# Kernel optimization log

Measured on AMD Instinct MI355X. Metric: run time of the kernel, lower is better.

Reference implementation:

```python
import jax, jax.numpy as jnp
import numpy as np

NUM_GROUPS = 32
EPS = 1e-6


def group_norm(x, gamma, beta):
    b, c, h, w = x.shape
    xg = x.reshape(b, NUM_GROUPS, c // NUM_GROUPS, h, w)
    mean = jnp.mean(xg, axis=(2, 3, 4), keepdims=True)
    var = jnp.var(xg, axis=(2, 3, 4), keepdims=True)
    xg = (xg - mean) * jax.lax.rsqrt(var + EPS)
    x = xg.reshape(b, c, h, w)
    return x * gamma[None, :, None, None] + beta[None, :, None, None]


def conv1x1(x, w, b):
    # x: [B,C,H,W], w: [Cout,Cin], b: [Cout]
    return jnp.einsum('bchw,oc->bohw', x, w) + b[None, :, None, None]


def setup_inputs() -> dict:
    key = jax.random.key(0)
    ks = jax.random.split(key, 11)
    B, C, H, W = 2, 512, 64, 64
    s = 1.0 / np.sqrt(C)
    return {
        'x': jax.random.normal(ks[0], (B, C, H, W), jnp.float32),
        'norm_gamma': jnp.ones((C,), jnp.float32),
        'norm_beta': jnp.zeros((C,), jnp.float32),
        'wq': jax.random.normal(ks[1], (C, C), jnp.float32) * s,
        'bq': jnp.zeros((C,), jnp.float32),
        'wk': jax.random.normal(ks[2], (C, C), jnp.float32) * s,
        'bk': jnp.zeros((C,), jnp.float32),
        'wv': jax.random.normal(ks[3], (C, C), jnp.float32) * s,
        'bv': jnp.zeros((C,), jnp.float32),
        'wo': jax.random.normal(ks[4], (C, C), jnp.float32) * s,
        'bo': jnp.zeros((C,), jnp.float32),
    }


def reference(x, norm_gamma, norm_beta, wq, bq, wk, bk, wv, bv, wo, bo):
    b, c, h, w = x.shape
    hn = group_norm(x, norm_gamma, norm_beta)
    q = conv1x1(hn, wq, bq).reshape(b, c, h * w)  # [B,C,HW]
    k = conv1x1(hn, wk, bk).reshape(b, c, h * w)
    v = conv1x1(hn, wv, bv).reshape(b, c, h * w)
    scale = jnp.asarray(c, x.dtype) ** -0.5
    # scores[b,i,j] = sum_c q[b,c,i] * k[b,c,j]
    scores = jnp.einsum('bci,bcj->bij', q, k) * scale
    attn = jax.nn.softmax(scores, axis=2)
    # out[b,c,i] = sum_j v[b,c,j] * attn[b,i,j]
    out = jnp.einsum('bcj,bij->bci', v, attn).reshape(b, c, h, w)
    out = conv1x1(out, wo, bo)
    return x + out
```

## Files before the change

kernel.cpp:

```cpp
#include <hip/hip_runtime.h>
#include <hip/hip_bf16.h>

using u16 = unsigned short;
typedef __attribute__((ext_vector_type(4))) float f32x4;
typedef __attribute__((ext_vector_type(8))) __bf16 bf16x8;
typedef __attribute__((ext_vector_type(8))) short s16x8;
typedef __attribute__((ext_vector_type(4))) short s16x4;

#define DEVI __device__ __forceinline__

constexpr int BATCH = 2, C = 512, HW = 4096, NG = 32, CPG = 16;

DEVI float b2f(u16 u) { union { unsigned u; float f; } a; a.u = ((unsigned)u) << 16; return a.f; }
DEVI u16 f2b(float f) {
  union { float f; unsigned u; } a; a.f = f;
  unsigned r = a.u + 0x7fffu + ((a.u >> 16) & 1u);
  return (u16)(r >> 16);
}

DEVI void xcd_remap(int& bx, int& by, int& bz) {
  const int nx = gridDim.x, ny = gridDim.y;
  const int nwg = nx * ny * gridDim.z;
  const int flat = blockIdx.x + nx * (blockIdx.y + ny * blockIdx.z);
  const int cpx = nwg >> 3;
  const int w = (flat & 7) * cpx + (flat >> 3);
  bx = w % nx;
  const int t = w / nx;
  by = t % ny;
  bz = t / ny;
}

__global__ __launch_bounds__(256) void cvt_w(const float* __restrict__ a, const float* __restrict__ b,
                                             const float* __restrict__ c, const float* __restrict__ d,
                                             u16* __restrict__ out) {
  int i = blockIdx.x * 256 + threadIdx.x;
  int w = i >> 16;
  int off = (i & 65535) * 4;
  const float* s = (w == 0) ? a : (w == 1) ? b : (w == 2) ? c : d;
  f32x4 v = *(const f32x4*)(s + off);
  s16x4 o;
  o[0] = (short)f2b(v[0]); o[1] = (short)f2b(v[1]); o[2] = (short)f2b(v[2]); o[3] = (short)f2b(v[3]);
  *(s16x4*)(out + (size_t)w * 262144 + off) = o;
}

__global__ __launch_bounds__(1024) void gn_stats(const float* __restrict__ x, float* __restrict__ stats) {
  int bg = blockIdx.x;
  const f32x4* xg = (const f32x4*)(x + (size_t)bg * (CPG * HW));
  float s = 0.f, ss = 0.f;
  for (int i = threadIdx.x; i < CPG * HW / 4; i += 1024) {
    f32x4 v = xg[i];
    s += v[0] + v[1] + v[2] + v[3];
    ss += v[0] * v[0] + v[1] * v[1] + v[2] * v[2] + v[3] * v[3];
  }
  #pragma unroll
  for (int o = 32; o; o >>= 1) { s += __shfl_xor(s, o); ss += __shfl_xor(ss, o); }
  __shared__ float red[32];
  int wv = threadIdx.x >> 6, ln = threadIdx.x & 63;
  if (ln == 0) { red[wv] = s; red[16 + wv] = ss; }
  __syncthreads();
  if (threadIdx.x == 0) {
    float S = 0.f, SS = 0.f;
    for (int i = 0; i < 16; ++i) { S += red[i]; SS += red[16 + i]; }
    float inv = 1.f / (float)(CPG * HW);
    float mean = S * inv;
    float var = SS * inv - mean * mean;
    stats[bg * 2] = mean;
    stats[bg * 2 + 1] = rsqrtf(var + 1e-6f);
  }
}

__global__ __launch_bounds__(256) void gn_normT(const float* __restrict__ x, const float* __restrict__ stats,
                                                const float* __restrict__ gamma, const float* __restrict__ beta,
                                                u16* __restrict__ hnT) {
  __shared__ u16 tile[64][66];
  int b = blockIdx.z, c0 = blockIdx.y * 64, h0 = blockIdx.x * 64;
  int t = threadIdx.x;
  const float* xb = x + ((size_t)b * C + c0) * HW + h0;
  int r = t / 16, cc = (t % 16) * 4;
  #pragma unroll
  for (int it = 0; it < 4; ++it) {
    int rr = it * 16 + r;
    int ch = c0 + rr;
    int g = b * NG + (ch >> 4);
    float mean = stats[g * 2], rstd = stats[g * 2 + 1];
    float ga = gamma[ch] * rstd;
    float be = beta[ch] - mean * ga;
    f32x4 v = *(const f32x4*)(xb + (size_t)rr * HW + cc);
    #pragma unroll
    for (int j = 0; j < 4; ++j) tile[rr][cc + j] = f2b(v[j] * ga + be);
  }
  __syncthreads();
  u16* op = hnT + (size_t)b * HW * C + (size_t)h0 * C + c0;
  int hr2 = t / 8, cg = (t % 8) * 8;
  #pragma unroll
  for (int it = 0; it < 2; ++it) {
    int hr = it * 32 + hr2;
    s16x8 o8;
    #pragma unroll
    for (int j = 0; j < 8; ++j) o8[j] = (short)tile[cg + j][hr];
    *(s16x8*)(op + (size_t)hr * C + cg) = o8;
  }
}

#define EPI_BIAS_M 1
#define EPI_BIAS_N 2
#define EPI_RESID  4
#define EPI_F32OUT 8
#define EPI_QK     32

template <int EPI>
__global__ __launch_bounds__(256) void gemm_bt(const u16* __restrict__ A, const u16* __restrict__ Bt,
                                               void* __restrict__ Co, int M, int N, int K,
                                               long long sA, long long sB, long long sC,
                                               const float* __restrict__ bias,
                                               const float* __restrict__ biasB,
                                               const float* __restrict__ resid, long long sR) {
  (void)M;
  __shared__ u16 ldsA[128 * 64];
  __shared__ u16 ldsB[128 * 64];
  const int tid = threadIdx.x;
  int bn, bm, bz;
  xcd_remap(bn, bm, bz);
  A += (size_t)bz * sA;
  Bt += (size_t)bz * sB;
  const int wave = tid >> 6, lane = tid & 63;
  const int wr = wave >> 1, wc = wave & 1;
  f32x4 acc[4][4] = {};

  const int srow = tid >> 3;
  const int sch = (tid & 7) ^ (srow & 7);
  const u16* gA = A + (size_t)(bm * 128 + srow) * K + sch * 8;
  const u16* gB = Bt + (size_t)(bn * 128 + srow) * K + sch * 8;
  u16* lA = ldsA + wave * 512;
  u16* lB = ldsB + wave * 512;

  for (int k0 = 0; k0 < K; k0 += 64) {
    #pragma unroll
    for (int cc = 0; cc < 4; ++cc) {
      __builtin_amdgcn_global_load_lds(
          (const __attribute__((address_space(1))) void*)(gA + (size_t)cc * 32 * K + k0),
          (__attribute__((address_space(3))) void*)(lA + cc * 2048), 16, 0, 0);
      __builtin_amdgcn_global_load_lds(
          (const __attribute__((address_space(1))) void*)(gB + (size_t)cc * 32 * K + k0),
          (__attribute__((address_space(3))) void*)(lB + cc * 2048), 16, 0, 0);
    }
    __syncthreads();
    #pragma unroll
    for (int kk = 0; kk < 2; ++kk) {
      bf16x8 af[4], bfv[4];
      #pragma unroll
      for (int m = 0; m < 4; ++m) {
        int r = wr * 64 + m * 16 + (lane & 15);
        int chunk = (kk * 4 + (lane >> 4)) ^ (r & 7);
        af[m] = *(const bf16x8*)(ldsA + r * 64 + chunk * 8);
      }
      #pragma unroll
      for (int n = 0; n < 4; ++n) {
        int r = wc * 64 + n * 16 + (lane & 15);
        int chunk = (kk * 4 + (lane >> 4)) ^ (r & 7);
        bfv[n] = *(const bf16x8*)(ldsB + r * 64 + chunk * 8);
      }
      #pragma unroll
      for (int m = 0; m < 4; ++m)
        #pragma unroll
        for (int n = 0; n < 4; ++n)
          acc[m][n] = __builtin_amdgcn_mfma_f32_16x16x32_bf16(af[m], bfv[n], acc[m][n], 0, 0, 0);
    }
    __syncthreads();
  }

  const int col0 = bn * 128 + wc * 64;
  const int row0 = bm * 128 + wr * 64 + ((lane >> 4) << 2);
  #pragma unroll
  for (int m = 0; m < 4; ++m) {
    #pragma unroll
    for (int j = 0; j < 4; ++j) {
      int gm = row0 + m * 16 + j;
      float bm_v = (EPI & EPI_BIAS_M) ? bias[gm] : 0.f;
      #pragma unroll
      for (int n = 0; n < 4; ++n) {
        int gn = col0 + n * 16 + (lane & 15);
        float v = acc[m][n][j] + bm_v;
        if (EPI & EPI_BIAS_N) {
          if (EPI & EPI_QK) v += (gn < 512) ? bias[gn] : biasB[gn - 512];
          else v += bias[gn];
        }
        if (EPI & EPI_RESID) v += resid[(size_t)bz * sR + (size_t)gm * N + gn];
        if (EPI & EPI_F32OUT)
          ((float*)Co)[(size_t)bz * sC + (size_t)gm * N + gn] = v;
        else
          ((u16*)Co)[(size_t)bz * sC + (size_t)gm * N + gn] = f2b(v);
      }
    }
  }
}

template <bool SCALED>
__global__ __launch_bounds__(512, 2) void gemm256(
    const u16* __restrict__ Ag, const u16* __restrict__ Bg,
    u16* __restrict__ Co, u16* __restrict__ Co2, int zSwitch,
    int Nld, int ldK, int nsplitLog, int kLen,
    long long sA, long long sB, long long sC, float scale) {
  __shared__ u16 lds[65536];
  const int tid = threadIdx.x;
  const int lane = tid & 63, w = tid >> 6;
  const int wm = w >> 2, wn = w & 3;
  const int l15 = lane & 15, l4 = lane >> 4;
  int bn, bm, z;
  xcd_remap(bn, bm, z);
  const int bz = z >> nsplitLog, kz = z & ((1 << nsplitLog) - 1);
  const int kStart = kz * kLen;
  const int NT = kLen >> 6;

  const int rStage = w * 8 + (lane >> 3);
  const int gch = (lane & 7) ^ (lane >> 3);
  const u16* gA = Ag + (size_t)bz * sA + (size_t)(bm * 256) * ldK + kStart + gch * 8;
  const u16* gB = Bg + (size_t)bz * sB + (size_t)(bn * 256) * ldK + kStart + gch * 8;

  f32x4 acc[8][4] = {};
  bf16x8 aF[4][2], bF[2][2][2];

  const int hB = wn >> 1, qB = wn & 1;
  const u16* pA0 = lds + (0 * 4 + wm) * 8192;
  const u16* pA1 = lds + (1 * 4 + wm) * 8192;
  const u16* pB0 = lds + (0 * 4 + 2 + hB) * 8192;
  const u16* pB1 = lds + (1 * 4 + 2 + hB) * 8192;

  #define STAGE(TT, DB, AB, HF) { \
    const u16* gbase = (AB) ? gB : gA; \
    u16* l0 = lds + ((DB) * 4 + (AB) * 2 + (HF)) * 8192 + w * 512; \
    _Pragma("unroll") for (int s = 0; s < 2; ++s) { \
      const u16* gp = gbase + (size_t)((HF) * 128 + s * 64 + rStage) * ldK + (TT) * 64; \
      __builtin_amdgcn_global_load_lds((const __attribute__((address_space(1))) void*)gp, \
          (__attribute__((address_space(3))) void*)(l0 + s * 4096), 16, 0, 0); } }

  #define LOAD_A(P, MH) { _Pragma("unroll") for (int j = 0; j < 4; ++j) \
    _Pragma("unroll") for (int kk = 0; kk < 2; ++kk) { \
      const int r_ = (MH) * 64 + j * 16 + l15; const int c_ = (kk * 4 + l4) ^ (r_ & 7); \
      aF[j][kk] = *(const bf16x8*)((P) + r_ * 64 + c_ * 8); } }

  #define LOAD_B(P, NH) { _Pragma("unroll") for (int j = 0; j < 2; ++j) \
    _Pragma("unroll") for (int kk = 0; kk < 2; ++kk) { \
      const int r_ = qB * 64 + (NH) * 32 + j * 16 + l15; const int c_ = (kk * 4 + l4) ^ (r_ & 7); \
      bF[NH][j][kk] = *(const bf16x8*)((P) + r_ * 64 + c_ * 8); } }

  #define MM(MH, NH) { __builtin_amdgcn_s_setprio(1); \
    _Pragma("unroll") for (int j = 0; j < 4; ++j) \
      _Pragma("unroll") for (int j2 = 0; j2 < 2; ++j2) \
        _Pragma("unroll") for (int kk = 0; kk < 2; ++kk) \
          acc[(MH) * 4 + j][(NH) * 2 + j2] = __builtin_amdgcn_mfma_f32_16x16x32_bf16( \
              aF[j][kk], bF[NH][j2][kk], acc[(MH) * 4 + j][(NH) * 2 + j2], 0, 0, 0); \
    __builtin_amdgcn_s_setprio(0); }

  #define BAR __builtin_amdgcn_s_barrier()
  #define WLG { asm volatile("s_waitcnt lgkmcnt(0)" ::: "memory"); __builtin_amdgcn_sched_barrier(0); }
  #define WV4 asm volatile("s_waitcnt vmcnt(4)" ::: "memory")
  #define WV0 asm volatile("s_waitcnt vmcnt(0)" ::: "memory")

  STAGE(0, 0, 1, 0); STAGE(0, 0, 1, 1);
  STAGE(0, 0, 0, 0); STAGE(0, 0, 0, 1);
  STAGE(1, 1, 1, 0); STAGE(1, 1, 1, 1);
  WV4; BAR;

  const int NI = NT / 2 - 1;
  for (int i = 0; i < NI; ++i) {
    const int t1 = 2 * i + 1, u0 = 2 * i + 2, u1 = 2 * i + 3;
    LOAD_A(pA0, 0); LOAD_B(pB0, 0); STAGE(t1, 1, 0, 0); BAR; WLG; MM(0, 0); BAR;
    LOAD_B(pB0, 1); STAGE(t1, 1, 0, 1); BAR; WLG; MM(0, 1); BAR;
    LOAD_A(pA0, 1); STAGE(u0, 0, 1, 0); BAR; WLG; MM(1, 1); BAR;
    STAGE(u0, 0, 1, 1); BAR; WLG; MM(1, 0); WV4; BAR;
    LOAD_A(pA1, 0); LOAD_B(pB1, 0); STAGE(u0, 0, 0, 0); BAR; WLG; MM(0, 0); BAR;
    LOAD_B(pB1, 1); STAGE(u0, 0, 0, 1); BAR; WLG; MM(0, 1); BAR;
    LOAD_A(pA1, 1); STAGE(u1, 1, 1, 0); BAR; WLG; MM(1, 1); BAR;
    STAGE(u1, 1, 1, 1); BAR; WLG; MM(1, 0); WV4; BAR;
  }
  {
    const int t1 = NT - 1;
    LOAD_A(pA0, 0); LOAD_B(pB0, 0); STAGE(t1, 1, 0, 0); BAR; WLG; MM(0, 0); BAR;
    LOAD_B(pB0, 1); STAGE(t1, 1, 0, 1); BAR; WLG; MM(0, 1); BAR;
    LOAD_A(pA0, 1); BAR; WLG; MM(1, 1); BAR;
    BAR; WLG; MM(1, 0); WV0; BAR;
    LOAD_A(pA1, 0); LOAD_B(pB1, 0); BAR; WLG; MM(0, 0); BAR;
    LOAD_B(pB1, 1); BAR; WLG; MM(0, 1); BAR;
    LOAD_A(pA1, 1); BAR; WLG; MM(1, 1); BAR;
    MM(1, 0);
  }
  #undef STAGE
  #undef LOAD_A
  #undef LOAD_B
  #undef MM
  #undef BAR
  #undef WLG
  #undef WV4
  #undef WV0

  {
    const int rloc = wm * 128 + l4 * 4;
    const int cloc = wn * 64 + l15;
    #pragma unroll
    for (int m = 0; m < 8; ++m) {
      #pragma unroll
      for (int j = 0; j < 4; ++j) {
        const int r_ = rloc + m * 16 + j;
        const int xr = ((r_ >> 2) & 3) << 5;
        #pragma unroll
        for (int n = 0; n < 4; ++n) {
          float v = acc[m][n][j];
          if (SCALED) v *= scale;
          *(u16*)((char*)lds + ((r_ * 512 + (cloc + n * 16) * 2) ^ xr)) = f2b(v);
        }
      }
    }
    __syncthreads();
    u16* outp = (z < zSwitch) ? (Co + (size_t)z * sC) : (Co2 + (size_t)(z - zSwitch) * sC);
    #pragma unroll
    for (int it = 0; it < 16; ++it) {
      const int idx = it * 512 + tid;
      const int r_ = idx >> 5, ch = idx & 31;
      const int xr = ((r_ >> 2) & 3) << 5;
      s16x8 d8 = *(const s16x8*)((const char*)lds + ((r_ * 512 + ch * 16) ^ xr));
      *(s16x8*)(outp + (size_t)(bm * 256 + r_) * Nld + bn * 256 + ch * 8) = d8;
    }
  }
}

__global__ __launch_bounds__(256) void softmax_rows(u16* __restrict__ S) {
  int row = blockIdx.x * 4 + (threadIdx.x >> 6);
  int lane = threadIdx.x & 63;
  s16x8* p = (s16x8*)(S + (size_t)row * 4096);
  float v[64];
  float m = -1e30f;
  #pragma unroll
  for (int j = 0; j < 8; ++j) {
    s16x8 raw = p[j * 64 + lane];
    #pragma unroll
    for (int e = 0; e < 8; ++e) {
      float f = b2f((u16)raw[e]);
      v[j * 8 + e] = f;
      m = fmaxf(m, f);
    }
  }
  #pragma unroll
  for (int o = 32; o; o >>= 1) m = fmaxf(m, __shfl_xor(m, o));
  float s = 0.f;
  #pragma unroll
  for (int i = 0; i < 64; ++i) { v[i] = __expf(v[i] - m); s += v[i]; }
  #pragma unroll
  for (int o = 32; o; o >>= 1) s += __shfl_xor(s, o);
  float r = 1.f / s;
  #pragma unroll
  for (int j = 0; j < 8; ++j) {
    s16x8 o8;
    #pragma unroll
    for (int e = 0; e < 8; ++e) o8[e] = (short)f2b(v[j * 8 + e] * r);
    p[j * 64 + lane] = o8;
  }
}

__global__ __launch_bounds__(256) void reduce_pv(const u16* __restrict__ P, const u16* __restrict__ P2,
                                                 u16* __restrict__ ao) {
  const size_t e = ((size_t)blockIdx.x * 256 + threadIdx.x) * 8;
  const int b = (int)(e >> 21);
  const size_t o = e & 2097151;
  float s[8] = {0.f, 0.f, 0.f, 0.f, 0.f, 0.f, 0.f, 0.f};
  #pragma unroll
  for (int kz = 0; kz < 4; ++kz) {
    const int zz = b * 4 + kz;
    const u16* src = (zz < 6) ? (P + (size_t)zz * 2097152) : (P2 + (size_t)(zz - 6) * 2097152);
    s16x8 v = *(const s16x8*)(src + o);
    #pragma unroll
    for (int j = 0; j < 8; ++j) s[j] += b2f((u16)v[j]);
  }
  s16x8 o8;
  #pragma unroll
  for (int j = 0; j < 8; ++j) o8[j] = (short)f2b(s[j]);
  *(s16x8*)(ao + e) = o8;
}

extern "C" void kernel_launch(void* const* d_in, const int* in_sizes, int n_in,
                              void* d_out, int out_size, void* d_ws, size_t ws_size,
                              hipStream_t stream) {
  (void)in_sizes; (void)n_in; (void)out_size; (void)ws_size;
  const float* x     = (const float*)d_in[0];
  const float* gamma = (const float*)d_in[1];
  const float* beta  = (const float*)d_in[2];
  const float* wq    = (const float*)d_in[3];
  const float* bq    = (const float*)d_in[4];
  const float* wk    = (const float*)d_in[5];
  const float* bk    = (const float*)d_in[6];
  const float* wv    = (const float*)d_in[7];
  const float* bv    = (const float*)d_in[8];
  const float* wo    = (const float*)d_in[9];
  const float* bo    = (const float*)d_in[10];

  char* ws = (char*)d_ws;
  const size_t MiB = 1024 * 1024;
  float* stats = (float*)ws;
  u16* wbf = (u16*)(ws + 1024);
  u16* vv  = (u16*)(ws + 4 * MiB);
  u16* qkT = (u16*)(ws + 12 * MiB);
  u16* hnT = (u16*)(ws + 28 * MiB);
  u16* Ppart = (u16*)(ws + 12 * MiB);
  u16* Sm  = (u16*)(ws + 36 * MiB);
  u16* aoT = (u16*)(ws + 36 * MiB);

  const long long sTok  = (long long)HW * C;
  const long long sTok2 = (long long)HW * 1024;
  const long long sS    = (long long)HW * HW;
  const float scale = 0.044194173824159216f;

  cvt_w<<<dim3(1024), dim3(256), 0, stream>>>(wq, wk, wv, wo, wbf);
  gn_stats<<<dim3(64), dim3(1024), 0, stream>>>(x, stats);
  gn_normT<<<dim3(HW / 64, C / 64, BATCH), dim3(256), 0, stream>>>(x, stats, gamma, beta, hnT);

  gemm_bt<EPI_BIAS_N | EPI_QK><<<dim3(8, 32, BATCH), dim3(256), 0, stream>>>(
      hnT, wbf, qkT, HW, 1024, C, sTok, 0, sTok2, bq, bk, nullptr, 0);
  gemm_bt<EPI_BIAS_M><<<dim3(32, 4, BATCH), dim3(256), 0, stream>>>(
      wbf + 2 * 262144, hnT, vv, C, HW, C, 0, sTok, sTok, bv, nullptr, nullptr, 0);

  gemm256<true><<<dim3(16, 16, BATCH), dim3(512), 0, stream>>>(
      qkT, qkT + 512, Sm, Sm, 1000, HW, 1024, 0, C, sTok2, sTok2, sS, scale);

  softmax_rows<<<dim3(2048), dim3(256), 0, stream>>>(Sm);

  gemm256<false><<<dim3(2, 16, BATCH * 4), dim3(512), 0, stream>>>(
      Sm, vv, Ppart, (u16*)d_out, 6, C, HW, 2, HW / 4, sS, sTok, (long long)2097152, 1.f);

  reduce_pv<<<dim3(2048), dim3(256), 0, stream>>>(Ppart, (const u16*)d_out, aoT);

  gemm_bt<EPI_BIAS_M | EPI_RESID | EPI_F32OUT><<<dim3(32, 4, BATCH), dim3(256), 0, stream>>>(
      wbf + 3 * 262144, aoT, d_out, C, HW, C, 0, sTok, (long long)C * HW, bo, nullptr, x, (long long)C * HW);
}
```

Before: 178.9 us.

## Split group-norm stats across more blocks with atomics; tweak gemm256 LDS waits

Group-norm statistics now use 512 small blocks instead of 64 large ones. Each block sums one eighth of a group and atomically adds its raw sum and sum of squares into stats, which cvt_w zeroes first. Mean and rstd are now computed inside gn_normT. Separately, the gemm256 main loop gets an extra partial lgkmcnt(8) wait before the first barrier of each phase, plus a __syncthreads before the epilogue reuses LDS. The aims are better GPU occupancy for the stats pass and safer LDS reuse, at the cost of atomic contention and run-to-run nondeterministic float summation.

```diff
diff --git a/kernel.cpp b/kernel.cpp
--- a/kernel.cpp
+++ b/kernel.cpp
@@ -32,7 +32,8 @@
 
 __global__ __launch_bounds__(256) void cvt_w(const float* __restrict__ a, const float* __restrict__ b,
                                              const float* __restrict__ c, const float* __restrict__ d,
-                                             u16* __restrict__ out) {
+                                             u16* __restrict__ out, float* __restrict__ stats) {
+  if (blockIdx.x == 0 && threadIdx.x < 128) stats[threadIdx.x] = 0.f;
   int i = blockIdx.x * 256 + threadIdx.x;
   int w = i >> 16;
   int off = (i & 65535) * 4;
@@ -43,29 +44,21 @@
   *(s16x4*)(out + (size_t)w * 262144 + off) = o;
 }
 
-__global__ __launch_bounds__(1024) void gn_stats(const float* __restrict__ x, float* __restrict__ stats) {
-  int bg = blockIdx.x;
-  const f32x4* xg = (const f32x4*)(x + (size_t)bg * (CPG * HW));
+__global__ __launch_bounds__(256) void gn_stats(const float* __restrict__ x, float* __restrict__ stats) {
+  const int bg = blockIdx.x >> 3, part = blockIdx.x & 7;
+  const f32x4* xg = (const f32x4*)(x + (size_t)bg * (CPG * HW)) + part * 2048;
   float s = 0.f, ss = 0.f;
-  for (int i = threadIdx.x; i < CPG * HW / 4; i += 1024) {
-    f32x4 v = xg[i];
+  #pragma unroll
+  for (int i = 0; i < 8; ++i) {
+    f32x4 v = xg[i * 256 + threadIdx.x];
     s += v[0] + v[1] + v[2] + v[3];
     ss += v[0] * v[0] + v[1] * v[1] + v[2] * v[2] + v[3] * v[3];
   }
   #pragma unroll
   for (int o = 32; o; o >>= 1) { s += __shfl_xor(s, o); ss += __shfl_xor(ss, o); }
-  __shared__ float red[32];
-  int wv = threadIdx.x >> 6, ln = threadIdx.x & 63;
-  if (ln == 0) { red[wv] = s; red[16 + wv] = ss; }
-  __syncthreads();
-  if (threadIdx.x == 0) {
-    float S = 0.f, SS = 0.f;
-    for (int i = 0; i < 16; ++i) { S += red[i]; SS += red[16 + i]; }
-    float inv = 1.f / (float)(CPG * HW);
-    float mean = S * inv;
-    float var = SS * inv - mean * mean;
-    stats[bg * 2] = mean;
-    stats[bg * 2 + 1] = rsqrtf(var + 1e-6f);
+  if ((threadIdx.x & 63) == 0) {
+    atomicAdd(&stats[bg * 2], s);
+    atomicAdd(&stats[bg * 2 + 1], ss);
   }
 }
 
@@ -77,12 +70,15 @@
   int t = threadIdx.x;
   const float* xb = x + ((size_t)b * C + c0) * HW + h0;
   int r = t / 16, cc = (t % 16) * 4;
+  const float inv = 1.f / (float)(CPG * HW);
   #pragma unroll
   for (int it = 0; it < 4; ++it) {
     int rr = it * 16 + r;
     int ch = c0 + rr;
     int g = b * NG + (ch >> 4);
-    float mean = stats[g * 2], rstd = stats[g * 2 + 1];
+    float S = stats[g * 2], SS = stats[g * 2 + 1];
+    float mean = S * inv;
+    float rstd = rsqrtf(SS * inv - mean * mean + 1e-6f);
     float ga = gamma[ch] * rstd;
     float be = beta[ch] - mean * ga;
     f32x4 v = *(const f32x4*)(xb + (size_t)rr * HW + cc);
@@ -254,6 +250,7 @@
 
   #define BAR __builtin_amdgcn_s_barrier()
   #define WLG { asm volatile("s_waitcnt lgkmcnt(0)" ::: "memory"); __builtin_amdgcn_sched_barrier(0); }
+  #define LG8 asm volatile("s_waitcnt lgkmcnt(8)" ::: "memory")
   #define WV4 asm volatile("s_waitcnt vmcnt(4)" ::: "memory")
   #define WV0 asm volatile("s_waitcnt vmcnt(0)" ::: "memory")
 
@@ -265,22 +262,22 @@
   const int NI = NT / 2 - 1;
   for (int i = 0; i < NI; ++i) {
     const int t1 = 2 * i + 1, u0 = 2 * i + 2, u1 = 2 * i + 3;
-    LOAD_A(pA0, 0); LOAD_B(pB0, 0); STAGE(t1, 1, 0, 0); BAR; WLG; MM(0, 0); BAR;
+    LOAD_A(pA0, 0); LOAD_B(pB0, 0); STAGE(t1, 1, 0, 0); LG8; BAR; WLG; MM(0, 0); BAR;
     LOAD_B(pB0, 1); STAGE(t1, 1, 0, 1); BAR; WLG; MM(0, 1); BAR;
     LOAD_A(pA0, 1); STAGE(u0, 0, 1, 0); BAR; WLG; MM(1, 1); BAR;
     STAGE(u0, 0, 1, 1); BAR; WLG; MM(1, 0); WV4; BAR;
-    LOAD_A(pA1, 0); LOAD_B(pB1, 0); STAGE(u0, 0, 0, 0); BAR; WLG; MM(0, 0); BAR;
+    LOAD_A(pA1, 0); LOAD_B(pB1, 0); STAGE(u0, 0, 0, 0); LG8; BAR; WLG; MM(0, 0); BAR;
     LOAD_B(pB1, 1); STAGE(u0, 0, 0, 1); BAR; WLG; MM(0, 1); BAR;
     LOAD_A(pA1, 1); STAGE(u1, 1, 1, 0); BAR; WLG; MM(1, 1); BAR;
     STAGE(u1, 1, 1, 1); BAR; WLG; MM(1, 0); WV4; BAR;
   }
   {
     const int t1 = NT - 1;
-    LOAD_A(pA0, 0); LOAD_B(pB0, 0); STAGE(t1, 1, 0, 0); BAR; WLG; MM(0, 0); BAR;
+    LOAD_A(pA0, 0); LOAD_B(pB0, 0); STAGE(t1, 1, 0, 0); LG8; BAR; WLG; MM(0, 0); BAR;
     LOAD_B(pB0, 1); STAGE(t1, 1, 0, 1); BAR; WLG; MM(0, 1); BAR;
     LOAD_A(pA0, 1); BAR; WLG; MM(1, 1); BAR;
     BAR; WLG; MM(1, 0); WV0; BAR;
-    LOAD_A(pA1, 0); LOAD_B(pB1, 0); BAR; WLG; MM(0, 0); BAR;
+    LOAD_A(pA1, 0); LOAD_B(pB1, 0); LG8; BAR; WLG; MM(0, 0); BAR;
     LOAD_B(pB1, 1); BAR; WLG; MM(0, 1); BAR;
     LOAD_A(pA1, 1); BAR; WLG; MM(1, 1); BAR;
     MM(1, 0);
@@ -291,9 +288,11 @@
   #undef MM
   #undef BAR
   #undef WLG
+  #undef LG8
   #undef WV4
   #undef WV0
 
+  __syncthreads();
   {
     const int rloc = wm * 128 + l4 * 4;
     const int cloc = wn * 64 + l15;
@@ -409,8 +408,8 @@
   const long long sS    = (long long)HW * HW;
   const float scale = 0.044194173824159216f;
 
-  cvt_w<<<dim3(1024), dim3(256), 0, stream>>>(wq, wk, wv, wo, wbf);
-  gn_stats<<<dim3(64), dim3(1024), 0, stream>>>(x, stats);
+  cvt_w<<<dim3(1024), dim3(256), 0, stream>>>(wq, wk, wv, wo, wbf, stats);
+  gn_stats<<<dim3(512), dim3(256), 0, stream>>>(x, stats);
   gn_normT<<<dim3(HW / 64, C / 64, BATCH), dim3(256), 0, stream>>>(x, stats, gamma, beta, hnT);
 
   gemm_bt<EPI_BIAS_N | EPI_QK><<<dim3(8, 32, BATCH), dim3(256), 0, stream>>>(
```

After: 185.9 us. 3.9% more time.
